# Kernel optimization log

Hardware: AMD Instinct MI355X
Metric: run time of the kernel (lower is better)

Reference implementation:

```python
import jax, jax.numpy as jnp
import numpy as np
from jax.scipy.special import erfc

CUTOFF = 10.0   # real-space cutoff (Angstrom)
ALPHA = 0.3     # Ewald splitting parameter (1/Angstrom)
KMAX = 8        # max integer k-index per dimension
N_ATOMS = 4096
BOX = 40.0      # cubic box edge (Angstrom)


def setup_inputs() -> dict:
    key = jax.random.key(0)
    kp, kq = jax.random.split(key)
    positions = jax.random.uniform(kp, (N_ATOMS, 3), dtype=jnp.float32) * BOX
    charges = jax.random.normal(kq, (N_ATOMS,), dtype=jnp.float32)
    charges = charges - charges.mean()  # enforce charge neutrality
    cell = jnp.eye(3, dtype=jnp.float32) * BOX  # row-vector lattice
    return {"positions": positions, "charges": charges, "cell": cell}


def _kvectors(kmax):
    # static integer grid (-kmax..kmax)^3 \\ {0}, built with numpy at trace time
    n = np.arange(-kmax, kmax + 1)
    grid = np.stack(np.meshgrid(n, n, n, indexing="ij"), axis=-1).reshape(-1, 3)
    grid = grid[np.any(grid != 0, axis=-1)]
    return jnp.asarray(grid, dtype=jnp.float32)  # [Nk, 3]


def _ewald(positions, charges, cell, cutoff, alpha, kmax):
    N = positions.shape[0]
    inv_cell = jnp.linalg.inv(cell)

    # ---- real-space sum: 0.5 * sum_{i!=j, r<rc} q_i q_j erfc(a r)/r (min image)
    rij = positions[:, None, :] - positions[None, :, :]          # [N,N,3]
    frac = rij @ inv_cell
    rij = (frac - jnp.round(frac)) @ cell                        # minimum image
    r2 = jnp.sum(rij * rij, axis=-1)                             # [N,N]
    eye = jnp.eye(N, dtype=bool)
    r = jnp.sqrt(jnp.where(eye, 1.0, r2))                        # safe sqrt on diag
    pair_mask = (~eye) & (r2 < cutoff * cutoff)
    qq = charges[:, None] * charges[None, :]
    e_real = 0.5 * jnp.sum(jnp.where(pair_mask, qq * erfc(alpha * r) / r, 0.0))

    # ---- reciprocal-space sum: (2pi/V) sum_k exp(-k^2/4a^2)/k^2 |S(k)|^2
    recip = 2.0 * jnp.pi * inv_cell.T                            # reciprocal lattice rows
    kvecs = _kvectors(kmax) @ recip                              # [Nk,3]
    k2 = jnp.sum(kvecs * kvecs, axis=-1)                         # [Nk]
    phase = positions @ kvecs.T                                  # [N,Nk]
    s_re = charges @ jnp.cos(phase)                              # [Nk]
    s_im = charges @ jnp.sin(phase)                              # [Nk]
    vol = jnp.abs(jnp.linalg.det(cell))
    coeff = jnp.exp(-k2 / (4.0 * alpha * alpha)) / k2
    e_recip = (2.0 * jnp.pi / vol) * jnp.sum(coeff * (s_re * s_re + s_im * s_im))

    # ---- self-energy correction
    e_self = -(alpha / jnp.sqrt(jnp.pi)) * jnp.sum(charges * charges)

    return e_real + e_recip + e_self


def reference(positions, charges, cell):
    return _ewald(positions, charges, cell, CUTOFF, ALPHA, KMAX)
```

## Files before the change

### kernel.cpp

```cpp
#include <hip/hip_runtime.h>
#include <math.h>

#define ALPHA 0.3f
#define KMAX 8
#define KDIM 17
#define KD2 (KDIM*KDIM)
#define NK_FULL (KDIM*KDIM*KDIM - 1)
#define NK_HALF (NK_FULL/2)
#define RECIP_KPB 16
#define NB_RECIP ((NK_HALF + RECIP_KPB - 1)/RECIP_KPB)
#define TWO_PI 6.28318530717958647692f

#define SELF_COEF (-0.16925687506432687f)
#define INV_4A2 (1.0f/(4.0f*ALPHA*ALPHA))
#define C1A (0.3275911f*ALPHA)
#define NA2 (-(ALPHA*ALPHA))

#define ITILE 256
#define JTILE 128

__device__ __forceinline__ void invert3x3(const float* __restrict__ c, float inv[9], float* det_out) {
    float a00=c[0],a01=c[1],a02=c[2];
    float a10=c[3],a11=c[4],a12=c[5];
    float a20=c[6],a21=c[7],a22=c[8];
    float c00 =  a11*a22 - a12*a21;
    float c01 = -(a10*a22 - a12*a20);
    float c02 =  a10*a21 - a11*a20;
    float det = a00*c00 + a01*c01 + a02*c02;
    float id = 1.0f/det;
    inv[0] =  c00*id;
    inv[1] = -(a01*a22 - a02*a21)*id;
    inv[2] =  (a01*a12 - a02*a11)*id;
    inv[3] =  c01*id;
    inv[4] =  (a00*a22 - a02*a20)*id;
    inv[5] = -(a00*a12 - a02*a10)*id;
    inv[6] =  c02*id;
    inv[7] = -(a00*a21 - a01*a20)*id;
    inv[8] =  (a00*a11 - a01*a10)*id;
    *det_out = det;
}

__device__ __forceinline__ float erfc_a(float r, float r2) {
    float t = __builtin_amdgcn_rcpf(fmaf(C1A, r, 1.0f));
    float p = t * fmaf(t, fmaf(t, fmaf(t, fmaf(t, 1.061405429f, -1.453152027f),
                       1.421413741f), -0.284496736f), 0.254829592f);
    return p * __expf(NA2 * r2);
}

__device__ __forceinline__ float block_reduce(float v) {
    for (int o = 32; o > 0; o >>= 1) v += __shfl_down(v, o, 64);
    __shared__ float smem[4];
    int lane = threadIdx.x & 63, wid = threadIdx.x >> 6;
    if (lane == 0) smem[wid] = v;
    __syncthreads();
    int nw = blockDim.x >> 6;
    v = ((int)threadIdx.x < nw) ? smem[threadIdx.x] : 0.0f;
    if (wid == 0) {
        for (int o = 4; o > 0; o >>= 1) v += __shfl_down(v, o, 64);
    }
    return v;
}

__global__ __launch_bounds__(256) void fused_kernel(const float* __restrict__ pos,
                                                    const float* __restrict__ q,
                                                    const float* __restrict__ cell,
                                                    float* __restrict__ e_out,
                                                    int N, int nb_recip, int nb_real) {
    __shared__ float4 tile[256];
    __shared__ float red_re[4][RECIP_KPB];
    __shared__ float red_im[4][RECIP_KPB];
    float inv[9]; float det;
    invert3x3(cell, inv, &det);
    bool ortho = (cell[1]==0.f) & (cell[2]==0.f) & (cell[3]==0.f) &
                 (cell[5]==0.f) & (cell[6]==0.f) & (cell[7]==0.f);

    int bid = blockIdx.x;
    int tid = threadIdx.x;
    int lane = tid & 63, wid = tid >> 6;

    if (bid < nb_recip) {
        int kbase = bid * RECIP_KPB;
        int kslot = tid & 15;
        int agrp  = tid >> 4;
        int kk = kbase + kslot;
        int kc = (kk < NK_HALF) ? kk : 0;
        float kx = (float)(kc / KD2 - KMAX);
        float ky = (float)((kc / KDIM) % KDIM - KMAX);
        float kz = (float)(kc % KDIM - KMAX);

        float sre = 0.0f, sim = 0.0f;
        for (int base = 0; base < N; base += 256) {
            int cnt = min(256, N - base);
            __syncthreads();
            if (tid < cnt) {
                int a = base + tid;
                float x = pos[3*a], y = pos[3*a+1], z = pos[3*a+2];
                float wx, wy, wz;
                if (ortho) { wx = x*inv[0]; wy = y*inv[4]; wz = z*inv[8]; }
                else {
                    wx = inv[0]*x + inv[3]*y + inv[6]*z;
                    wy = inv[1]*x + inv[4]*y + inv[7]*z;
                    wz = inv[2]*x + inv[5]*y + inv[8]*z;
                }
                tile[tid] = make_float4(wx, wy, wz, q[a]);
            }
            __syncthreads();
            int s0 = agrp * 16, s1 = min(s0 + 16, cnt);
            #pragma unroll 4
            for (int t = s0; t < s1; ++t) {
                float4 w = tile[t];
                float ph = fmaf(kx, w.x, fmaf(ky, w.y, kz * w.z));
                ph -= rintf(ph);
                sre = fmaf(w.w, __builtin_amdgcn_cosf(ph), sre);
                sim = fmaf(w.w, __builtin_amdgcn_sinf(ph), sim);
            }
        }
        sre += __shfl_xor(sre, 16, 64);  sim += __shfl_xor(sim, 16, 64);
        sre += __shfl_xor(sre, 32, 64);  sim += __shfl_xor(sim, 32, 64);
        if (lane < RECIP_KPB) { red_re[wid][kslot] = sre; red_im[wid][kslot] = sim; }
        __syncthreads();
        if (wid == 0) {
            float e = 0.0f;
            if (lane < RECIP_KPB) {
                float sr = red_re[0][lane] + red_re[1][lane] + red_re[2][lane] + red_re[3][lane];
                float si = red_im[0][lane] + red_im[1][lane] + red_im[2][lane] + red_im[3][lane];
                int t = kbase + lane;
                if (t < NK_HALF) {
                    float nx = (float)(t / KD2 - KMAX);
                    float ny = (float)((t / KDIM) % KDIM - KMAX);
                    float nz = (float)(t % KDIM - KMAX);
                    float kvx = TWO_PI * (nx*inv[0] + ny*inv[1] + nz*inv[2]);
                    float kvy = TWO_PI * (nx*inv[3] + ny*inv[4] + nz*inv[5]);
                    float kvz = TWO_PI * (nx*inv[6] + ny*inv[7] + nz*inv[8]);
                    float k2 = fmaf(kvx, kvx, fmaf(kvy, kvy, kvz * kvz));
                    float vol = fabsf(det);
                    float pref = 2.0f * (TWO_PI / vol);
                    float coeff = __expf(-k2 * INV_4A2) * __builtin_amdgcn_rcpf(k2);
                    e = pref * coeff * fmaf(sr, sr, si * si);
                }
            }
            for (int o = 8; o > 0; o >>= 1) e += __shfl_down(e, o, 64);
            if (lane == 0) unsafeAtomicAdd(e_out, e);
        }
        if (bid == nb_recip - 1) {
            float fa = 0.0f;
            for (int t = tid; t < N; t += 256) {
                float qt = q[t];
                fa = fmaf(SELF_COEF * qt, qt, fa);
            }
            __syncthreads();
            float s2 = block_reduce(fa);
            if (tid == 0) unsafeAtomicAdd(e_out, s2);
        }
    } else {
        int rbid = bid - nb_recip;
        int bi = 0, acc = 0;
        for (;;) {
            int up = min(N, (bi + 1) * ITILE);
            int nc = (up + JTILE - 1) / JTILE;
            if (rbid < acc + nc) break;
            acc += nc; ++bi;
        }
        int bj = rbid - acc;

        float c0 = cell[0], c4 = cell[4], c8 = cell[8];
        float c1 = cell[1], c2 = cell[2], c3 = cell[3];
        float c5 = cell[5], c6 = cell[6], c7 = cell[7];

        int ibase = bi * ITILE;
        int i = ibase + tid;
        bool ivalid = (i < N);
        float xi = 0.f, yi = 0.f, zi = 0.f, qi = 0.f;
        if (ivalid) { xi = pos[3*i]; yi = pos[3*i+1]; zi = pos[3*i+2]; qi = q[i]; }

        int jbase = bj * JTILE;
        int jcount = min(JTILE, N - jbase);
        if (tid < jcount) {
            int j = jbase + tid;
            tile[tid] = make_float4(pos[3*j], pos[3*j+1], pos[3*j+2], q[j]);
        }
        __syncthreads();

        bool full = (jbase + JTILE <= ibase) && (ibase + ITILE <= N) && (jcount == JTILE);

        float acc_e = 0.0f;
        if (ortho) {
            float i0 = inv[0], i4 = inv[4], i8 = inv[8];
            if (full) {
                #pragma unroll 8
                for (int t = 0; t < JTILE; ++t) {
                    float4 p = tile[t];
                    float dx = xi - p.x, dy = yi - p.y, dz = zi - p.z;
                    float rx = fmaf(-c0, rintf(dx * i0), dx);
                    float ry = fmaf(-c4, rintf(dy * i4), dy);
                    float rz = fmaf(-c8, rintf(dz * i8), dz);
                    float r2 = fmaf(rx, rx, fmaf(ry, ry, rz * rz));
                    float rinv = __builtin_amdgcn_rsqf(r2);
                    float r = r2 * rinv;
                    acc_e = fmaf(p.w * rinv, erfc_a(r, r2), acc_e);
                }
            } else {
                #pragma unroll 8
                for (int t = 0; t < jcount; ++t) {
                    float4 p = tile[t];
                    float dx = xi - p.x, dy = yi - p.y, dz = zi - p.z;
                    float rx = fmaf(-c0, rintf(dx * i0), dx);
                    float ry = fmaf(-c4, rintf(dy * i4), dy);
                    float rz = fmaf(-c8, rintf(dz * i8), dz);
                    float r2 = fmaf(rx, rx, fmaf(ry, ry, rz * rz));
                    float rinv = __builtin_amdgcn_rsqf(r2);
                    float r = r2 * rinv;
                    float val = p.w * rinv * erfc_a(r, r2);
                    bool ok = ivalid && ((jbase + t) < i);
                    acc_e += ok ? val : 0.0f;
                }
            }
        } else {
            #pragma unroll 4
            for (int t = 0; t < jcount; ++t) {
                float4 p = tile[t];
                float dx = xi - p.x, dy = yi - p.y, dz = zi - p.z;
                float fx = dx*inv[0] + dy*inv[3] + dz*inv[6];
                float fy = dx*inv[1] + dy*inv[4] + dz*inv[7];
                float fz = dx*inv[2] + dy*inv[5] + dz*inv[8];
                fx -= rintf(fx); fy -= rintf(fy); fz -= rintf(fz);
                float rx = fx*c0 + fy*c3 + fz*c6;
                float ry = fx*c1 + fy*c4 + fz*c7;
                float rz = fx*c2 + fy*c5 + fz*c8;
                float r2 = fmaf(rx, rx, fmaf(ry, ry, rz * rz));
                float rinv = __builtin_amdgcn_rsqf(r2);
                float r = r2 * rinv;
                float val = p.w * rinv * erfc_a(r, r2);
                bool ok = ivalid && ((jbase + t) < i);
                acc_e += ok ? val : 0.0f;
            }
        }
        acc_e *= qi;

        float s = block_reduce(acc_e);
        if (tid == 0) unsafeAtomicAdd(e_out, s);
    }
}

extern "C" void kernel_launch(void* const* d_in, const int* in_sizes, int n_in,
                              void* d_out, int out_size, void* d_ws, size_t ws_size,
                              hipStream_t stream) {
    const float* pos  = (const float*)d_in[0];
    const float* q    = (const float*)d_in[1];
    const float* cell = (const float*)d_in[2];
    int N = in_sizes[1];
    float* e_out = (float*)d_out;

    int nbi = (N + ITILE - 1) / ITILE;
    int nb_real = 0;
    for (int bi = 0; bi < nbi; ++bi) {
        int up = (N < (bi + 1) * ITILE) ? N : (bi + 1) * ITILE;
        nb_real += (up + JTILE - 1) / JTILE;
    }
    int nb_recip = NB_RECIP;

    hipMemsetAsync(e_out, 0, sizeof(float), stream);

    fused_kernel<<<nb_recip + nb_real, 256, 0, stream>>>(pos, q, cell, e_out,
                                                         N, nb_recip, nb_real);
}
```

Baseline: 78.88 us.

## Double-buffer reciprocal atom tiles and split accumulators in both loops

The reciprocal-space loop now uses two shared tiles. Each round loads the next 256 atoms into registers while computing on the current tile, which removes one barrier per round and overlaps global loads with the sin/cos work. Both the reciprocal and the real-space inner loops use several independent accumulators (2 and 4) to break the serial FMA dependency chains and expose more instruction-level parallelism. This costs extra shared memory and registers, which may reduce occupancy, and it changes the order of the floating-point summation.

```diff
diff --git a/kernel.cpp b/kernel.cpp
--- a/kernel.cpp
+++ b/kernel.cpp
@@ -47,6 +47,19 @@
     return p * __expf(NA2 * r2);
 }
 
+__device__ __forceinline__ float pair_ortho(float4 p, float xi, float yi, float zi,
+                                            float i0, float i4, float i8,
+                                            float c0, float c4, float c8) {
+    float dx = xi - p.x, dy = yi - p.y, dz = zi - p.z;
+    float rx = fmaf(-c0, rintf(dx * i0), dx);
+    float ry = fmaf(-c4, rintf(dy * i4), dy);
+    float rz = fmaf(-c8, rintf(dz * i8), dz);
+    float r2 = fmaf(rx, rx, fmaf(ry, ry, rz * rz));
+    float rinv = __builtin_amdgcn_rsqf(r2);
+    float r = r2 * rinv;
+    return p.w * rinv * erfc_a(r, r2);
+}
+
 __device__ __forceinline__ float block_reduce(float v) {
     for (int o = 32; o > 0; o >>= 1) v += __shfl_down(v, o, 64);
     __shared__ float smem[4];
@@ -66,7 +79,7 @@
                                                     const float* __restrict__ cell,
                                                     float* __restrict__ e_out,
                                                     int N, int nb_recip, int nb_real) {
-    __shared__ float4 tile[256];
+    __shared__ float4 tile2[2][256];
     __shared__ float red_re[4][RECIP_KPB];
     __shared__ float red_im[4][RECIP_KPB];
     float inv[9]; float det;
@@ -88,12 +101,31 @@
         float ky = (float)((kc / KDIM) % KDIM - KMAX);
         float kz = (float)(kc % KDIM - KMAX);
 
-        float sre = 0.0f, sim = 0.0f;
-        for (int base = 0; base < N; base += 256) {
+        int nrounds = (N + 255) >> 8;
+
+        if (tid < N) {
+            int a = tid;
+            float x = pos[3*a], y = pos[3*a+1], z = pos[3*a+2];
+            float wx, wy, wz;
+            if (ortho) { wx = x*inv[0]; wy = y*inv[4]; wz = z*inv[8]; }
+            else {
+                wx = inv[0]*x + inv[3]*y + inv[6]*z;
+                wy = inv[1]*x + inv[4]*y + inv[7]*z;
+                wz = inv[2]*x + inv[5]*y + inv[8]*z;
+            }
+            tile2[0][tid] = make_float4(wx, wy, wz, q[a]);
+        }
+        __syncthreads();
+
+        float sre0 = 0.0f, sim0 = 0.0f, sre1 = 0.0f, sim1 = 0.0f;
+        for (int r = 0; r < nrounds; ++r) {
+            int base = r << 8;
             int cnt = min(256, N - base);
-            __syncthreads();
-            if (tid < cnt) {
-                int a = base + tid;
+            int abase = base + 256;
+            bool pf = (abase + tid) < N;
+            float4 nxt = make_float4(0.f, 0.f, 0.f, 0.f);
+            if (pf) {
+                int a = abase + tid;
                 float x = pos[3*a], y = pos[3*a+1], z = pos[3*a+2];
                 float wx, wy, wz;
                 if (ortho) { wx = x*inv[0]; wy = y*inv[4]; wz = z*inv[8]; }
@@ -102,19 +134,36 @@
                     wy = inv[1]*x + inv[4]*y + inv[7]*z;
                     wz = inv[2]*x + inv[5]*y + inv[8]*z;
                 }
-                tile[tid] = make_float4(wx, wy, wz, q[a]);
-            }
-            __syncthreads();
-            int s0 = agrp * 16, s1 = min(s0 + 16, cnt);
+                nxt = make_float4(wx, wy, wz, q[a]);
+            }
+            const float4* buf = tile2[r & 1];
+            int s0 = agrp * 16;
+            int s1 = min(s0 + 16, cnt);
+            int t = s0;
             #pragma unroll 4
-            for (int t = s0; t < s1; ++t) {
-                float4 w = tile[t];
+            for (; t + 1 < s1; t += 2) {
+                float4 w0 = buf[t], w1 = buf[t + 1];
+                float ph0 = fmaf(kx, w0.x, fmaf(ky, w0.y, kz * w0.z));
+                float ph1 = fmaf(kx, w1.x, fmaf(ky, w1.y, kz * w1.z));
+                ph0 -= rintf(ph0);
+                ph1 -= rintf(ph1);
+                sre0 = fmaf(w0.w, __builtin_amdgcn_cosf(ph0), sre0);
+                sim0 = fmaf(w0.w, __builtin_amdgcn_sinf(ph0), sim0);
+                sre1 = fmaf(w1.w, __builtin_amdgcn_cosf(ph1), sre1);
+                sim1 = fmaf(w1.w, __builtin_amdgcn_sinf(ph1), sim1);
+            }
+            for (; t < s1; ++t) {
+                float4 w = buf[t];
                 float ph = fmaf(kx, w.x, fmaf(ky, w.y, kz * w.z));
                 ph -= rintf(ph);
-                sre = fmaf(w.w, __builtin_amdgcn_cosf(ph), sre);
-                sim = fmaf(w.w, __builtin_amdgcn_sinf(ph), sim);
-            }
-        }
+                sre0 = fmaf(w.w, __builtin_amdgcn_cosf(ph), sre0);
+                sim0 = fmaf(w.w, __builtin_amdgcn_sinf(ph), sim0);
+            }
+            if (pf) tile2[(r + 1) & 1][tid] = nxt;
+            __syncthreads();
+        }
+        float sre = sre0 + sre1, sim = sim0 + sim1;
+
         sre += __shfl_xor(sre, 16, 64);  sim += __shfl_xor(sim, 16, 64);
         sre += __shfl_xor(sre, 32, 64);  sim += __shfl_xor(sim, 32, 64);
         if (lane < RECIP_KPB) { red_re[wid][kslot] = sre; red_im[wid][kslot] = sim; }
@@ -175,6 +224,7 @@
 
         int jbase = bj * JTILE;
         int jcount = min(JTILE, N - jbase);
+        float4* tile = tile2[0];
         if (tid < jcount) {
             int j = jbase + tid;
             tile[tid] = make_float4(pos[3*j], pos[3*j+1], pos[3*j+2], q[j]);
@@ -183,40 +233,43 @@
 
         bool full = (jbase + JTILE <= ibase) && (ibase + ITILE <= N) && (jcount == JTILE);
 
-        float acc_e = 0.0f;
+        float e0 = 0.0f, e1 = 0.0f, e2 = 0.0f, e3 = 0.0f;
         if (ortho) {
             float i0 = inv[0], i4 = inv[4], i8 = inv[8];
             if (full) {
-                #pragma unroll 8
-                for (int t = 0; t < JTILE; ++t) {
+                #pragma unroll 2
+                for (int t = 0; t < JTILE; t += 4) {
+                    float4 p0 = tile[t+0], p1 = tile[t+1], p2 = tile[t+2], p3 = tile[t+3];
+                    e0 += pair_ortho(p0, xi, yi, zi, i0, i4, i8, c0, c4, c8);
+                    e1 += pair_ortho(p1, xi, yi, zi, i0, i4, i8, c0, c4, c8);
+                    e2 += pair_ortho(p2, xi, yi, zi, i0, i4, i8, c0, c4, c8);
+                    e3 += pair_ortho(p3, xi, yi, zi, i0, i4, i8, c0, c4, c8);
+                }
+            } else {
+                int t = 0;
+                for (; t + 3 < jcount; t += 4) {
+                    float4 p0 = tile[t+0], p1 = tile[t+1], p2 = tile[t+2], p3 = tile[t+3];
+                    float v0 = pair_ortho(p0, xi, yi, zi, i0, i4, i8, c0, c4, c8);
+                    float v1 = pair_ortho(p1, xi, yi, zi, i0, i4, i8, c0, c4, c8);
+                    float v2 = pair_ortho(p2, xi, yi, zi, i0, i4, i8, c0, c4, c8);
+                    float v3 = pair_ortho(p3, xi, yi, zi, i0, i4, i8, c0, c4, c8);
+                    bool k0 = ivalid && ((jbase + t + 0) < i);
+                    bool k1 = ivalid && ((jbase + t + 1) < i);
+                    bool k2 = ivalid && ((jbase + t + 2) < i);
+                    bool k3 = ivalid && ((jbase + t + 3) < i);
+                    e0 += k0 ? v0 : 0.0f;
+                    e1 += k1 ? v1 : 0.0f;
+                    e2 += k2 ? v2 : 0.0f;
+                    e3 += k3 ? v3 : 0.0f;
+                }
+                for (; t < jcount; ++t) {
                     float4 p = tile[t];
-                    float dx = xi - p.x, dy = yi - p.y, dz = zi - p.z;
-                    float rx = fmaf(-c0, rintf(dx * i0), dx);
-                    float ry = fmaf(-c4, rintf(dy * i4), dy);
-                    float rz = fmaf(-c8, rintf(dz * i8), dz);
-                    float r2 = fmaf(rx, rx, fmaf(ry, ry, rz * rz));
-                    float rinv = __builtin_amdgcn_rsqf(r2);
-                    float r = r2 * rinv;
-                    acc_e = fmaf(p.w * rinv, erfc_a(r, r2), acc_e);
-                }
-            } else {
-                #pragma unroll 8
-                for (int t = 0; t < jcount; ++t) {
-                    float4 p = tile[t];
-                    float dx = xi - p.x, dy = yi - p.y, dz = zi - p.z;
-                    float rx = fmaf(-c0, rintf(dx * i0), dx);
-                    float ry = fmaf(-c4, rintf(dy * i4), dy);
-                    float rz = fmaf(-c8, rintf(dz * i8), dz);
-                    float r2 = fmaf(rx, rx, fmaf(ry, ry, rz * rz));
-                    float rinv = __builtin_amdgcn_rsqf(r2);
-                    float r = r2 * rinv;
-                    float val = p.w * rinv * erfc_a(r, r2);
+                    float v = pair_ortho(p, xi, yi, zi, i0, i4, i8, c0, c4, c8);
                     bool ok = ivalid && ((jbase + t) < i);
-                    acc_e += ok ? val : 0.0f;
+                    e0 += ok ? v : 0.0f;
                 }
             }
         } else {
-            #pragma unroll 4
             for (int t = 0; t < jcount; ++t) {
                 float4 p = tile[t];
                 float dx = xi - p.x, dy = yi - p.y, dz = zi - p.z;
@@ -232,10 +285,10 @@
                 float r = r2 * rinv;
                 float val = p.w * rinv * erfc_a(r, r2);
                 bool ok = ivalid && ((jbase + t) < i);
-                acc_e += ok ? val : 0.0f;
-            }
-        }
-        acc_e *= qi;
+                e0 += ok ? val : 0.0f;
+            }
+        }
+        float acc_e = ((e0 + e1) + (e2 + e3)) * qi;
 
         float s = block_reduce(acc_e);
         if (tid == 0) unsafeAtomicAdd(e_out, s);
```

New measurement: 78.16 us. No clear change (-0.9%).
